# Kernel optimization log

Hardware: AMD Instinct MI355X
Metric: run time of the kernel (lower is better)

The kernel has to match this reference:

```python
import jax, jax.numpy as jnp
import numpy as np

SEGMENT_LENGTHS = [1024, 2048, 4096]
DILATION_RATES = [1, 2, 4]


def setup_inputs() -> dict:
    key = jax.random.key(0)
    kq, kk, kv = jax.random.split(key, 3)
    shape = (2, 4096, 12, 64)  # (batch, seq_len, num_heads, head_dim)
    return {
        "q": jax.random.normal(kq, shape, dtype=jnp.float32),
        "k": jax.random.normal(kk, shape, dtype=jnp.float32),
        "v": jax.random.normal(kv, shape, dtype=jnp.float32),
        "is_causal": 0,
    }


def _group_attention(qg, kg, vg, L, dil_rate, is_causal, scale):
    # qg/kg/vg: [b, n, hg, d]; block-local attention with block size L.
    # NOTE: the original _get_dilated_indices degenerates to the identity
    # segment slice (i=0 row fills all L indices before truncation), so the
    # dilated gather equals the contiguous segment for any dilation_rate.
    b, n, hg, d = qg.shape
    ns = n // L
    q_ = qg.reshape(b, ns, L, hg, d)
    k_ = kg.reshape(b, ns, L, hg, d)
    v_ = vg.reshape(b, ns, L, hg, d)
    scores = jnp.einsum("bsqhd,bskhd->bshqk", q_, k_) * scale  # [b,ns,hg,L,L]
    if is_causal and dil_rate == 1:
        # causal mask is applied only to segment 0 in the original
        causal = jnp.tril(jnp.ones((L, L), dtype=bool))  # [L,L]
        seg0 = (jnp.arange(ns) == 0)[None, :, None, None, None]  # [1,ns,1,1,1]
        neg = jnp.asarray(jnp.finfo(scores.dtype).min, scores.dtype)
        scores = jnp.where(seg0 & ~causal[None, None, None], neg, scores)
    attn = jax.nn.softmax(scores, axis=-1)
    out = jnp.einsum("bshqk,bskhd->bsqhd", attn, v_)
    return out.reshape(b, n, hg, d)


def reference(q, k, v, is_causal):
    b, n, h, d = q.shape
    num_groups = len(SEGMENT_LENGTHS)
    hg = h // num_groups
    scale = 1.0 / (float(d) ** 0.5)
    outs = []
    for gi, (L, r) in enumerate(zip(SEGMENT_LENGTHS, DILATION_RATES)):
        hs = gi * hg
        he = (gi + 1) * hg if gi < num_groups - 1 else h
        outs.append(
            _group_attention(
                q[:, :, hs:he], k[:, :, hs:he], v[:, :, hs:he],
                L, r, bool(is_causal), scale,
            )
        )
    return jnp.concatenate(outs, axis=2)  # [b, n, h, d]
```

## Files before the change

### kernel.cpp

```cpp
#include <hip/hip_runtime.h>
#include <hip/hip_bf16.h>

typedef __bf16 bf16;
typedef _Float16 f16;
typedef __attribute__((ext_vector_type(2))) __bf16 bf16x2;
typedef __attribute__((ext_vector_type(4))) __bf16 bf16x4;
typedef __attribute__((ext_vector_type(8))) __bf16 bf16x8;
typedef __attribute__((ext_vector_type(4))) _Float16 f16x4;
typedef __attribute__((ext_vector_type(8))) _Float16 f16x8;
typedef __attribute__((ext_vector_type(4))) float f32x4;
typedef __attribute__((ext_vector_type(16))) float f32x16;
typedef __attribute__((ext_vector_type(4))) unsigned u32x4;

#define SW(row, col) ((col) ^ (((row) & 7) << 3))

#define GL16(g, l) __builtin_amdgcn_global_load_lds( \
    (const __attribute__((address_space(1))) void*)(g), \
    (__attribute__((address_space(3))) void*)(l), 16, 0, 0)

static __device__ __forceinline__ unsigned pkbf(float a, float b) {
    bf16x2 t = { (bf16)a, (bf16)b };
    return __builtin_bit_cast(unsigned, t);
}

__global__ __launch_bounds__(256) void prep_fused(
    const float* __restrict__ k, const float* __restrict__ v,
    bf16* __restrict__ Kb, bf16* __restrict__ Vt)
{
    __shared__ bf16 T[64][72];
    const int bid = (int)blockIdx.x;
    const int tid = threadIdx.x;
    if (bid < 6144) {
        const size_t i = ((size_t)bid * 256 + tid) * 4;
        float4 f = *(const float4*)(k + i);
        bf16x4 o = { (bf16)f.x, (bf16)f.y, (bf16)f.z, (bf16)f.w };
        *(bf16x4*)(Kb + i) = o;
        return;
    }
    const int vb  = bid - 6144;
    const int n64 = vb & 63;
    const int bh  = vb >> 6;
    const int b   = bh / 12, h = bh - b * 12;
    {
        const int i  = tid >> 2;
        const int dc = (tid & 3) << 4;
        const float* vp = v + (size_t)(b * 4096 + (n64 << 6) + i) * 768 + h * 64 + dc;
        float tv[16];
#pragma unroll
        for (int j2 = 0; j2 < 4; ++j2) *(float4*)&tv[j2 * 4] = ((const float4*)vp)[j2];
#pragma unroll
        for (int j = 0; j < 16; ++j) T[dc + j][i] = (bf16)tv[j];
    }
    __syncthreads();
    {
        const int d  = tid >> 2;
        const int nc = (tid & 3) << 4;
        bf16* op = Vt + (size_t)(bh * 64 + d) * 4096 + (n64 << 6) + nc;
        *(bf16x8*)op       = *(const bf16x8*)&T[d][nc];
        *(bf16x8*)(op + 8) = *(const bf16x8*)&T[d][nc + 8];
    }
}

__global__ __launch_bounds__(256, 3) void attn_kv32(
    const float* __restrict__ q, const bf16* __restrict__ Kb,
    const bf16* __restrict__ Vt, const int* __restrict__ causal_p,
    float* __restrict__ out, f16* __restrict__ Opart, float* __restrict__ lpart)
{
    __shared__ bf16 Ksh[2][32][64];
    __shared__ bf16 Vsh[2][64][32];

    const int tid  = threadIdx.x;
    const int lane = tid & 63;
    const int w    = tid >> 6;
    const int l31  = lane & 31;
    const int h5   = lane >> 5;

    const int bid = (int)blockIdx.x;
    int h, b, qc, so, sp = 0, lbase = 0, oslot = 0;
    bool direct = false, cflag = false;
    if (bid < 1024) {
        h = 8 + (bid >> 8);
        const int r = bid & 255; sp = r >> 6;
        const int r2 = r & 63; b = r2 >> 5; qc = r2 & 31;
        so = sp << 10;
        const int gi = (h - 8) * 64 + b * 32 + qc;
        lbase = gi * 4; oslot = gi * 3 + (sp - 1);
    } else if (bid < 1536) {
        const int i = bid - 1024;
        h = 4 + (i >> 7);
        const int r = i & 127; sp = r >> 6;
        const int r2 = r & 63; b = r2 >> 5; qc = r2 & 31;
        so = ((qc >> 4) << 11) + (sp << 10);
        const int gi = (h - 4) * 64 + b * 32 + qc;
        lbase = 1024 + gi * 2; oslot = 768 + gi;
    } else {
        const int i = bid - 1536;
        h = i >> 6;
        const int r = i & 63; b = r >> 5; qc = r & 31;
        so = (qc >> 3) << 10; direct = true; cflag = true;
    }
    const int q0 = qc << 7;
    const bool causal = cflag && ((qc >> 3) == 0) && (*causal_p != 0);
    const int qg = q0 + (w << 5) + l31;

    const float QS = 0.125f * 1.44269504088896340736f;
    const float* qrp = q + (size_t)(b * 4096 + qg) * 768 + h * 64 + (h5 << 3);
    bf16x8 qf[4];
#pragma unroll
    for (int c = 0; c < 4; ++c) {
        float tq[8];
        *(float4*)&tq[0] = *(const float4*)(qrp + 16 * c);
        *(float4*)&tq[4] = *(const float4*)(qrp + 16 * c + 4);
        bf16x8 t;
#pragma unroll
        for (int j = 0; j < 8; ++j) t[j] = (bf16)(tq[j] * QS);
        qf[c] = t;
    }

    f32x16 o0 = (f32x16)(0.f), o1 = (f32x16)(0.f);
    float lreg = 0.f;

    const int rk  = tid >> 3;
    const int gk  = (tid & 7) ^ (rk & 7);
    const int dv  = tid >> 2;
    const int gv  = (tid & 3) ^ (dv & 3);
    const bf16* kp = Kb + (size_t)(b * 4096 + so + rk) * 768 + h * 64 + gk * 8;
    const bf16* vp = Vt + (size_t)((b * 12 + h) * 64 + dv) * 4096 + so + gv * 8;

    {
        GL16(kp, &Ksh[0][w << 3][0]);
        GL16(vp, &Vsh[0][w << 4][0]);
        kp += 32 * 768; vp += 32;
    }

    for (int t = 0; t < 32; ++t) {
        const int buf = t & 1;
        __builtin_amdgcn_s_barrier();
        if (t < 31) {
            GL16(kp, &Ksh[buf ^ 1][w << 3][0]);
            GL16(vp, &Vsh[buf ^ 1][w << 4][0]);
            kp += 32 * 768; vp += 32;
            asm volatile("s_waitcnt vmcnt(2)" ::: "memory");
        } else {
            asm volatile("s_waitcnt vmcnt(0)" ::: "memory");
        }
        __builtin_amdgcn_s_barrier();

        const bf16 (*Kc)[64] = Ksh[buf];
        const bf16 (*Vc)[32] = Vsh[buf];

        f32x16 s0 = (f32x16)(-12.0f);
        __builtin_amdgcn_s_setprio(1);
#pragma unroll
        for (int c = 0; c < 4; ++c) {
            const int col = (c << 4) + (h5 << 3);
            bf16x8 kf = *(const bf16x8*)&Kc[l31][SW(l31, col)];
            s0 = __builtin_amdgcn_mfma_f32_32x32x16_bf16(kf, qf[c], s0, 0, 0, 0);
        }
        __builtin_amdgcn_s_setprio(0);

        if (causal) {
#pragma unroll
            for (int reg = 0; reg < 16; ++reg) {
                const int kr = (reg & 3) + ((reg >> 2) << 3) + (h5 << 2);
                if (so + (t << 5) + kr > qg) s0[reg] = -1e30f;
            }
        }

        float rs0 = 0.f, rs1 = 0.f;
#pragma unroll
        for (int reg = 0; reg < 16; ++reg) {
            s0[reg] = __builtin_amdgcn_exp2f(s0[reg]);
            if (reg & 1) rs1 += s0[reg]; else rs0 += s0[reg];
        }
        lreg += rs0 + rs1;

        unsigned pk[4][2];
#pragma unroll
        for (int g = 0; g < 4; ++g) {
            pk[g][0] = pkbf(s0[4 * g + 0], s0[4 * g + 1]);
            pk[g][1] = pkbf(s0[4 * g + 2], s0[4 * g + 3]);
        }
        bf16x8 pf[2];
#pragma unroll
        for (int c = 0; c < 2; ++c) {
            unsigned X0 = pk[2 * c][0],     X1 = pk[2 * c][1];
            unsigned Y0 = pk[2 * c + 1][0], Y1 = pk[2 * c + 1][1];
            asm("v_permlane32_swap_b32 %0, %1" : "+v"(X0), "+v"(Y0));
            asm("v_permlane32_swap_b32 %0, %1" : "+v"(X1), "+v"(Y1));
            u32x4 fu = { X0, X1, Y0, Y1 };
            pf[c] = __builtin_bit_cast(bf16x8, fu);
        }

        __builtin_amdgcn_s_setprio(1);
#pragma unroll
        for (int c = 0; c < 2; ++c) {
            const int col = (c << 4) + (h5 << 3);
            bf16x8 vf0 = *(const bf16x8*)&Vc[l31][col ^ ((l31 & 3) << 3)];
            bf16x8 vf1 = *(const bf16x8*)&Vc[32 + l31][col ^ ((l31 & 3) << 3)];
            o0 = __builtin_amdgcn_mfma_f32_32x32x16_bf16(vf0, pf[c], o0, 0, 0, 0);
            o1 = __builtin_amdgcn_mfma_f32_32x32x16_bf16(vf1, pf[c], o1, 0, 0, 0);
        }
        __builtin_amdgcn_s_setprio(0);
    }

    const float lt = lreg + __shfl_xor(lreg, 32);
    const int qloc = (w << 5) + l31;
    if (direct) {
        const float inv = 1.0f / lt;
        float* op = out + (size_t)(b * 4096 + q0 + qloc) * 768 + h * 64;
#pragma unroll
        for (int rr = 0; rr < 4; ++rr) {
            const int d0 = (rr << 3) + (h5 << 2);
            float4 a = { o0[4 * rr] * inv, o0[4 * rr + 1] * inv, o0[4 * rr + 2] * inv, o0[4 * rr + 3] * inv };
            float4 c = { o1[4 * rr] * inv, o1[4 * rr + 1] * inv, o1[4 * rr + 2] * inv, o1[4 * rr + 3] * inv };
            *(float4*)&op[d0]      = a;
            *(float4*)&op[32 + d0] = c;
        }
    } else {
        if (h5 == 0) lpart[(size_t)(lbase + sp) * 128 + qloc] = lt;
        if (sp == 0) {
            float* op = out + (size_t)(b * 4096 + q0 + qloc) * 768 + h * 64;
#pragma unroll
            for (int rr = 0; rr < 4; ++rr) {
                const int d0 = (rr << 3) + (h5 << 2);
                float4 a = { o0[4 * rr], o0[4 * rr + 1], o0[4 * rr + 2], o0[4 * rr + 3] };
                float4 c = { o1[4 * rr], o1[4 * rr + 1], o1[4 * rr + 2], o1[4 * rr + 3] };
                *(float4*)&op[d0]      = a;
                *(float4*)&op[32 + d0] = c;
            }
        } else {
            f16* os = Opart + (size_t)oslot * 8192 + qloc * 64;
#pragma unroll
            for (int rr = 0; rr < 4; ++rr) {
                const int d0 = (rr << 3) + (h5 << 2);
                f16x4 a = { (f16)o0[4 * rr], (f16)o0[4 * rr + 1], (f16)o0[4 * rr + 2], (f16)o0[4 * rr + 3] };
                f16x4 c = { (f16)o1[4 * rr], (f16)o1[4 * rr + 1], (f16)o1[4 * rr + 2], (f16)o1[4 * rr + 3] };
                *(f16x4*)&os[d0]      = a;
                *(f16x4*)&os[32 + d0] = c;
            }
        }
    }
}

__global__ __launch_bounds__(256) void reduce_multi(
    const f16* __restrict__ Opart, const float* __restrict__ lpart,
    float* __restrict__ out)
{
    const int g = (int)blockIdx.x;
    int h, b, qc, nsp, lbase, sbase, nslots;
    if (g < 256) {
        h = 8 + (g >> 6); b = (g >> 5) & 1; qc = g & 31;
        nsp = 4; lbase = g * 4; sbase = g * 3; nslots = 3;
    } else {
        const int gi = g - 256;
        h = 4 + (gi >> 6); b = (gi >> 5) & 1; qc = gi & 31;
        nsp = 2; lbase = 1024 + gi * 2; sbase = 768 + gi; nslots = 1;
    }
    const int t = threadIdx.x;
    const int row = t >> 1;
    const int dh = (t & 1) << 5;
    float l = 0.f;
    for (int s = 0; s < nsp; ++s) l += lpart[(size_t)(lbase + s) * 128 + row];
    const float inv = 1.0f / l;
    float* op = out + (size_t)(b * 4096 + (qc << 7) + row) * 768 + h * 64 + dh;
#pragma unroll
    for (int j = 0; j < 32; j += 8) {
        float acc[8];
        float4 a0 = *(const float4*)(op + j);
        float4 a1 = *(const float4*)(op + j + 4);
        acc[0] = a0.x; acc[1] = a0.y; acc[2] = a0.z; acc[3] = a0.w;
        acc[4] = a1.x; acc[5] = a1.y; acc[6] = a1.z; acc[7] = a1.w;
        for (int s = 0; s < nslots; ++s) {
            f16x8 c = *(const f16x8*)(Opart + (size_t)(sbase + s) * 8192 + row * 64 + dh + j);
#pragma unroll
            for (int e = 0; e < 8; ++e) acc[e] += (float)c[e];
        }
        float4 r0 = { acc[0] * inv, acc[1] * inv, acc[2] * inv, acc[3] * inv };
        float4 r1 = { acc[4] * inv, acc[5] * inv, acc[6] * inv, acc[7] * inv };
        *(float4*)(op + j)     = r0;
        *(float4*)(op + j + 4) = r1;
    }
}

__global__ __launch_bounds__(256, 3) void dila_attn32(
    const float* __restrict__ q, const bf16* __restrict__ Kb,
    const bf16* __restrict__ Vt, const int* __restrict__ causal_p,
    float* __restrict__ out, f16* __restrict__ Opart, float* __restrict__ lpart)
{
    __shared__ bf16 Ksh[2][64][64];
    __shared__ bf16 Vsh[2][64][64];

    const int tid  = threadIdx.x;
    const int lane = tid & 63;
    const int w    = tid >> 6;
    const int l31  = lane & 31;
    const int h5   = lane >> 5;

    const int bid = (int)blockIdx.x;
    int h, b, qc, so, nt, sp = 0, gslot = -1;
    bool cflag = false;
    if (bid < 512) {
        h = 8 + (bid >> 7);
        const int r = bid & 127; sp = r >> 6;
        const int r2 = r & 63; b = r2 >> 5; qc = r2 & 31;
        so = sp << 11; nt = 32;
        gslot = (h - 8) * 64 + b * 32 + qc;
    } else if (bid < 768) {
        const int i = bid - 512;
        h = 4 + (i >> 6);
        const int r = i & 63; b = r >> 5; qc = r & 31;
        so = (qc >> 4) << 11; nt = 32;
    } else {
        const int i = bid - 768;
        h = i >> 7;
        const int r = i & 127; sp = r >> 6;
        const int r2 = r & 63; b = r2 >> 5; qc = r2 & 31;
        so = ((qc >> 3) << 10) + (sp << 9); nt = 8; cflag = true;
        gslot = 256 + h * 64 + b * 32 + qc;
    }
    const int q0 = qc << 7;
    const bool causal = cflag && ((qc >> 3) == 0) && (*causal_p != 0);
    const int qg = q0 + (w << 5) + l31;

    const float QS = 0.125f * 1.44269504088896340736f;
    const float* qrp = q + (size_t)(b * 4096 + qg) * 768 + h * 64 + (h5 << 3);
    bf16x8 qf[4];
#pragma unroll
    for (int c = 0; c < 4; ++c) {
        float tq[8];
        *(float4*)&tq[0] = *(const float4*)(qrp + 16 * c);
        *(float4*)&tq[4] = *(const float4*)(qrp + 16 * c + 4);
        bf16x8 t;
#pragma unroll
        for (int j = 0; j < 8; ++j) t[j] = (bf16)(tq[j] * QS);
        qf[c] = t;
    }

    f32x16 o0 = (f32x16)(0.f), o1 = (f32x16)(0.f);
    float lreg = 0.f;

    const int rK = lane >> 3;
    const int gK = (lane & 7) ^ rK;
    const bf16* kp = Kb + (size_t)(b * 4096 + so + (w << 4) + rK) * 768 + h * 64 + gK * 8;
    const bf16* vp = Vt + (size_t)((b * 12 + h) * 64 + (w << 4) + rK) * 4096 + so + gK * 8;

    {
        bf16* kd = &Ksh[0][w << 4][0];
        bf16* vd = &Vsh[0][w << 4][0];
        GL16(kp, kd); GL16(kp + 8 * 768, kd + 512);
        GL16(vp, vd); GL16(vp + 8 * 4096, vd + 512);
        kp += 64 * 768; vp += 64;
    }

    for (int t = 0; t < nt; ++t) {
        const int buf = t & 1;
        __builtin_amdgcn_s_barrier();
        if (t + 1 < nt) {
            bf16* kd = &Ksh[buf ^ 1][w << 4][0];
            bf16* vd = &Vsh[buf ^ 1][w << 4][0];
            GL16(kp, kd); GL16(kp + 8 * 768, kd + 512);
            GL16(vp, vd); GL16(vp + 8 * 4096, vd + 512);
            kp += 64 * 768; vp += 64;
            asm volatile("s_waitcnt vmcnt(4)" ::: "memory");
        } else {
            asm volatile("s_waitcnt vmcnt(0)" ::: "memory");
        }
        __builtin_amdgcn_s_barrier();

        const bf16 (*Kc)[64] = Ksh[buf];
        const bf16 (*Vc)[64] = Vsh[buf];

        f32x16 s0 = (f32x16)(-12.0f), s1 = (f32x16)(-12.0f);
        __builtin_amdgcn_s_setprio(1);
#pragma unroll
        for (int c = 0; c < 4; ++c) {
            const int col = (c << 4) + (h5 << 3);
            bf16x8 kf0 = *(const bf16x8*)&Kc[l31][SW(l31, col)];
            bf16x8 kf1 = *(const bf16x8*)&Kc[32 + l31][SW(32 + l31, col)];
            s0 = __builtin_amdgcn_mfma_f32_32x32x16_bf16(kf0, qf[c], s0, 0, 0, 0);
            s1 = __builtin_amdgcn_mfma_f32_32x32x16_bf16(kf1, qf[c], s1, 0, 0, 0);
        }
        __builtin_amdgcn_s_setprio(0);

        if (causal) {
#pragma unroll
            for (int reg = 0; reg < 16; ++reg) {
                const int kr = (reg & 3) + ((reg >> 2) << 3) + (h5 << 2);
                if (so + (t << 6) + kr > qg)      s0[reg] = -1e30f;
                if (so + (t << 6) + 32 + kr > qg) s1[reg] = -1e30f;
            }
        }

        float p0[16], p1[16], rs = 0.f;
#pragma unroll
        for (int reg = 0; reg < 16; ++reg) {
            p0[reg] = __builtin_amdgcn_exp2f(s0[reg]);
            p1[reg] = __builtin_amdgcn_exp2f(s1[reg]);
            rs += p0[reg] + p1[reg];
        }
        lreg += rs;

        unsigned pk[8][2];
#pragma unroll
        for (int rr = 0; rr < 4; ++rr) {
            pk[rr][0]     = pkbf(p0[4 * rr + 0], p0[4 * rr + 1]);
            pk[rr][1]     = pkbf(p0[4 * rr + 2], p0[4 * rr + 3]);
            pk[4 + rr][0] = pkbf(p1[4 * rr + 0], p1[4 * rr + 1]);
            pk[4 + rr][1] = pkbf(p1[4 * rr + 2], p1[4 * rr + 3]);
        }
        bf16x8 pf[4];
#pragma unroll
        for (int c = 0; c < 4; ++c) {
            unsigned X0 = pk[2 * c][0],     X1 = pk[2 * c][1];
            unsigned Y0 = pk[2 * c + 1][0], Y1 = pk[2 * c + 1][1];
            asm("v_permlane32_swap_b32 %0, %1" : "+v"(X0), "+v"(Y0));
            asm("v_permlane32_swap_b32 %0, %1" : "+v"(X1), "+v"(Y1));
            u32x4 fu = { X0, X1, Y0, Y1 };
            pf[c] = __builtin_bit_cast(bf16x8, fu);
        }

        __builtin_amdgcn_s_setprio(1);
#pragma unroll
        for (int c = 0; c < 4; ++c) {
            const int col = (c << 4) + (h5 << 3);
            bf16x8 vf0 = *(const bf16x8*)&Vc[l31][SW(l31, col)];
            bf16x8 vf1 = *(const bf16x8*)&Vc[32 + l31][SW(32 + l31, col)];
            o0 = __builtin_amdgcn_mfma_f32_32x32x16_bf16(vf0, pf[c], o0, 0, 0, 0);
            o1 = __builtin_amdgcn_mfma_f32_32x32x16_bf16(vf1, pf[c], o1, 0, 0, 0);
        }
        __builtin_amdgcn_s_setprio(0);
    }

    const float lt = lreg + __shfl_xor(lreg, 32);
    const int qloc = (w << 5) + l31;
    if (gslot < 0) {
        const float inv = 1.0f / lt;
        float* op = out + (size_t)(b * 4096 + q0 + qloc) * 768 + h * 64;
#pragma unroll
        for (int rr = 0; rr < 4; ++rr) {
            const int d0 = (rr << 3) + (h5 << 2);
            float4 a = { o0[4 * rr] * inv, o0[4 * rr + 1] * inv, o0[4 * rr + 2] * inv, o0[4 * rr + 3] * inv };
            float4 c = { o1[4 * rr] * inv, o1[4 * rr + 1] * inv, o1[4 * rr + 2] * inv, o1[4 * rr + 3] * inv };
            *(float4*)&op[d0]      = a;
            *(float4*)&op[32 + d0] = c;
        }
    } else if (sp == 0) {
        float* op = out + (size_t)(b * 4096 + q0 + qloc) * 768 + h * 64;
#pragma unroll
        for (int rr = 0; rr < 4; ++rr) {
            const int d0 = (rr << 3) + (h5 << 2);
            float4 a = { o0[4 * rr], o0[4 * rr + 1], o0[4 * rr + 2], o0[4 * rr + 3] };
            float4 c = { o1[4 * rr], o1[4 * rr + 1], o1[4 * rr + 2], o1[4 * rr + 3] };
            *(float4*)&op[d0]      = a;
            *(float4*)&op[32 + d0] = c;
        }
        if (h5 == 0) lpart[gslot * 256 + qloc] = lt;
    } else {
        f16* os = Opart + (size_t)gslot * 8192 + qloc * 64;
#pragma unroll
        for (int rr = 0; rr < 4; ++rr) {
            const int d0 = (rr << 3) + (h5 << 2);
            f16x4 a = { (f16)o0[4 * rr], (f16)o0[4 * rr + 1], (f16)o0[4 * rr + 2], (f16)o0[4 * rr + 3] };
            f16x4 c = { (f16)o1[4 * rr], (f16)o1[4 * rr + 1], (f16)o1[4 * rr + 2], (f16)o1[4 * rr + 3] };
            *(f16x4*)&os[d0]      = a;
            *(f16x4*)&os[32 + d0] = c;
        }
        if (h5 == 0) lpart[gslot * 256 + 128 + qloc] = lt;
    }
}

__global__ __launch_bounds__(256) void reduce_splits(
    const f16* __restrict__ Opart, const float* __restrict__ lpart,
    float* __restrict__ out)
{
    const int g = (int)blockIdx.x;
    int h, b, qc;
    if (g < 256) { h = 8 + (g >> 6); b = (g >> 5) & 1; qc = g & 31; }
    else { const int g2 = g - 256; h = g2 >> 6; b = (g2 >> 5) & 1; qc = g2 & 31; }
    const int t = threadIdx.x;
    const int row = t >> 1;
    const int dh = (t & 1) << 5;
    const f16* s1 = Opart + (size_t)g * 8192 + row * 64 + dh;
    const float inv = 1.0f / (lpart[g * 256 + row] + lpart[g * 256 + 128 + row]);
    float* op = out + (size_t)(b * 4096 + (qc << 7) + row) * 768 + h * 64 + dh;
#pragma unroll
    for (int j = 0; j < 32; j += 8) {
        float4 a0 = *(const float4*)(op + j);
        float4 a1 = *(const float4*)(op + j + 4);
        f16x8 c = *(const f16x8*)(s1 + j);
        float4 r0 = { (a0.x + (float)c[0]) * inv, (a0.y + (float)c[1]) * inv,
                      (a0.z + (float)c[2]) * inv, (a0.w + (float)c[3]) * inv };
        float4 r1 = { (a1.x + (float)c[4]) * inv, (a1.y + (float)c[5]) * inv,
                      (a1.z + (float)c[6]) * inv, (a1.w + (float)c[7]) * inv };
        *(float4*)(op + j)     = r0;
        *(float4*)(op + j + 4) = r1;
    }
}

__global__ __launch_bounds__(256) void dila_attn_legacy(
    const float* __restrict__ q, const float* __restrict__ k,
    const float* __restrict__ v, const int* __restrict__ causal_p,
    float* __restrict__ out)
{
    __shared__ bf16 Ksh[64][64];
    __shared__ bf16 Vsh[64][64];
    __shared__ bf16 Psh[4][16][72];

    const int tid  = threadIdx.x;
    const int lane = tid & 63;
    const int wid  = tid >> 6;
    const int lm   = lane & 15;
    const int lg   = lane >> 4;

    const int h   = 11 - (int)(blockIdx.x >> 7);
    const int rem = (int)(blockIdx.x & 127);
    const int b   = rem >> 6;
    const int qb  = rem & 63;

    const int grp = h >> 2;
    const int L   = 1024 << grp;
    const int q0  = qb << 6;
    const int seg = q0 / L;
    const int kv0 = seg * L;
    const int nt  = L >> 6;
    const bool causal = (grp == 0) && (seg == 0) && (*causal_p != 0);

    const float* qb_p = q   + (size_t)b * 4096 * 768 + h * 64;
    const float* kb_p = k   + (size_t)b * 4096 * 768 + h * 64;
    const float* vb_p = v   + (size_t)b * 4096 * 768 + h * 64;
    float*       ob_p = out + (size_t)b * 4096 * 768 + h * 64;

    const float QSCALE = 0.125f * 1.44269504088896340736f;
    const int qrow = q0 + (wid << 4) + lm;
    const float* qp = qb_p + (size_t)qrow * 768 + (lg << 3);
    bf16x8 qf[2];
#pragma unroll
    for (int kc = 0; kc < 2; ++kc) {
        float tq[8];
        *(float4*)&tq[0] = ((const float4*)(qp + kc * 32))[0];
        *(float4*)&tq[4] = ((const float4*)(qp + kc * 32))[1];
        bf16x8 tt;
#pragma unroll
        for (int j = 0; j < 8; ++j) tt[j] = (bf16)(tq[j] * QSCALE);
        qf[kc] = tt;
    }

    f32x4 o[4];
#pragma unroll
    for (int i = 0; i < 4; ++i) o[i] = (f32x4){0.f, 0.f, 0.f, 0.f};
    float mrun = -1e30f, lrun = 0.f;

    const int sr = tid >> 2;
    const int sc = (tid & 3) << 4;
    const int vbr = tid >> 4;
    const int vbc = tid & 15;

    const float* kp0 = kb_p + (size_t)(kv0 + sr) * 768 + sc;
    const float* vp0 = vb_p + (size_t)(kv0 + (vbr << 2)) * 768 + (vbc << 2);

    for (int t = 0; t < nt; ++t) {
        {
            const float* kp = kp0 + (size_t)t * (64 * 768);
            float tk[16];
#pragma unroll
            for (int i = 0; i < 4; ++i) *(float4*)&tk[4 * i] = ((const float4*)kp)[i];
            bf16x8 c0, c1;
#pragma unroll
            for (int j = 0; j < 8; ++j) { c0[j] = (bf16)tk[j]; c1[j] = (bf16)tk[8 + j]; }
            *(bf16x8*)&Ksh[sr][SW(sr, sc)]     = c0;
            *(bf16x8*)&Ksh[sr][SW(sr, sc + 8)] = c1;
        }
        {
            const float* vp = vp0 + (size_t)t * (64 * 768);
            float4 tv[4];
#pragma unroll
            for (int i = 0; i < 4; ++i) tv[i] = *(const float4*)(vp + (size_t)i * 768);
#pragma unroll
            for (int jc = 0; jc < 4; ++jc) {
                const int d = (vbc << 2) + jc;
                bf16x4 wv = { (bf16)((&tv[0].x)[jc]), (bf16)((&tv[1].x)[jc]),
                              (bf16)((&tv[2].x)[jc]), (bf16)((&tv[3].x)[jc]) };
                *(bf16x4*)&Vsh[d][SW(d, vbr << 2)] = wv;
            }
        }
        __syncthreads();

        f32x4 s[4];
#pragma unroll
        for (int cb = 0; cb < 4; ++cb) {
            f32x4 acc = (f32x4){0.f, 0.f, 0.f, 0.f};
            const int krow = (cb << 4) + lm;
#pragma unroll
            for (int kc = 0; kc < 2; ++kc) {
                bf16x8 kf = *(const bf16x8*)&Ksh[krow][SW(krow, (lg << 3) + (kc << 5))];
                acc = __builtin_amdgcn_mfma_f32_16x16x32_bf16(kf, qf[kc], acc, 0, 0, 0);
            }
            s[cb] = acc;
        }

        if (causal) {
            const int qg = q0 + (wid << 4) + lm;
#pragma unroll
            for (int cb = 0; cb < 4; ++cb) {
                const int kbase = kv0 + (t << 6) + (cb << 4) + (lg << 2);
#pragma unroll
                for (int r = 0; r < 4; ++r)
                    if (kbase + r > qg) s[cb][r] = -1e30f;
            }
        }

        {
            float mx = fmaxf(fmaxf(fmaxf(s[0][0], s[0][1]), fmaxf(s[0][2], s[0][3])),
                             fmaxf(fmaxf(s[1][0], s[1][1]), fmaxf(s[1][2], s[1][3])));
            float mx2 = fmaxf(fmaxf(fmaxf(s[2][0], s[2][1]), fmaxf(s[2][2], s[2][3])),
                              fmaxf(fmaxf(s[3][0], s[3][1]), fmaxf(s[3][2], s[3][3])));
            mx = fmaxf(mx, mx2);
            mx = fmaxf(mx, __shfl_xor(mx, 16));
            mx = fmaxf(mx, __shfl_xor(mx, 32));
            const float mn = fmaxf(mrun, mx);
            const float cr = __builtin_amdgcn_exp2f(mrun - mn);
            mrun = mn;
            float rs = 0.f;
#pragma unroll
            for (int cb = 0; cb < 4; ++cb) {
                f32x4 pp;
#pragma unroll
                for (int r = 0; r < 4; ++r) {
                    pp[r] = __builtin_amdgcn_exp2f(s[cb][r] - mn);
                    rs += pp[r];
                }
                bf16x4 wv = { (bf16)pp[0], (bf16)pp[1], (bf16)pp[2], (bf16)pp[3] };
                *(bf16x4*)&Psh[wid][lm][(cb << 4) + (lg << 2)] = wv;
            }
            rs += __shfl_xor(rs, 16);
            rs += __shfl_xor(rs, 32);
            lrun = lrun * cr + rs;
#pragma unroll
            for (int db = 0; db < 4; ++db)
#pragma unroll
                for (int r = 0; r < 4; ++r) o[db][r] *= cr;
        }

        {
            bf16x8 pfr[2];
#pragma unroll
            for (int kc = 0; kc < 2; ++kc)
                pfr[kc] = *(const bf16x8*)&Psh[wid][lm][(lg << 3) + (kc << 5)];
#pragma unroll
            for (int db = 0; db < 4; ++db) {
                const int vr = (db << 4) + lm;
#pragma unroll
                for (int kc = 0; kc < 2; ++kc) {
                    bf16x8 vf = *(const bf16x8*)&Vsh[vr][SW(vr, (lg << 3) + (kc << 5))];
                    o[db] = __builtin_amdgcn_mfma_f32_16x16x32_bf16(vf, pfr[kc], o[db], 0, 0, 0);
                }
            }
        }
        __syncthreads();
    }

    {
        const float inv = 1.0f / lrun;
        const int orow = q0 + (wid << 4) + lm;
        float* op = ob_p + (size_t)orow * 768 + (lg << 2);
#pragma unroll
        for (int db = 0; db < 4; ++db) {
            float4 wv = { o[db][0] * inv, o[db][1] * inv, o[db][2] * inv, o[db][3] * inv };
            *(float4*)(op + (db << 4)) = wv;
        }
    }
}

extern "C" void kernel_launch(void* const* d_in, const int* in_sizes, int n_in,
                              void* d_out, int out_size, void* d_ws, size_t ws_size,
                              hipStream_t stream) {
    const float* q = (const float*)d_in[0];
    const float* k = (const float*)d_in[1];
    const float* v = (const float*)d_in[2];
    const int* causal_p = (const int*)d_in[3];
    float* out = (float*)d_out;

    const size_t elems = (size_t)2 * 4096 * 12 * 64;
    const size_t kb_b  = elems * sizeof(bf16);
    const size_t vt_b  = elems * sizeof(bf16);

    const size_t opP_b = (size_t)1024 * 8192 * sizeof(f16);
    const size_t lpP_b = (size_t)1536 * 128 * sizeof(float);
    const size_t needP = kb_b + vt_b + opP_b + lpP_b;

    const size_t opF_b = (size_t)512 * 8192 * sizeof(f16);
    const size_t lpF_b = (size_t)512 * 256 * sizeof(float);
    const size_t needF = kb_b + vt_b + opF_b + lpF_b;

    if (ws_size >= needP) {
        bf16* Kb    = (bf16*)d_ws;
        bf16* Vt    = Kb + elems;
        f16*  Opart = (f16*)(Vt + elems);
        float* lpart = (float*)((char*)Opart + opP_b);
        prep_fused<<<dim3(7680), dim3(256), 0, stream>>>(k, v, Kb, Vt);
        attn_kv32<<<dim3(1792), dim3(256), 0, stream>>>(q, Kb, Vt, causal_p, out, Opart, lpart);
        reduce_multi<<<dim3(512), dim3(256), 0, stream>>>(Opart, lpart, out);
    } else if (ws_size >= needF) {
        bf16* Kb    = (bf16*)d_ws;
        bf16* Vt    = Kb + elems;
        f16*  Opart = (f16*)(Vt + elems);
        float* lpart = (float*)((char*)Opart + opF_b);
        prep_fused<<<dim3(7680), dim3(256), 0, stream>>>(k, v, Kb, Vt);
        dila_attn32<<<dim3(1280), dim3(256), 0, stream>>>(q, Kb, Vt, causal_p, out, Opart, lpart);
        reduce_splits<<<dim3(512), dim3(256), 0, stream>>>(Opart, lpart, out);
    } else {
        dila_attn_legacy<<<dim3(1536), dim3(256), 0, stream>>>(q, k, v, causal_p, out);
    }
}
```

Measured before the change: 114.2 us.

## Pre-pack K/V into MFMA fragment layout and drop LDS staging in attention

The prep kernel now writes K and V in a layout already arranged as per-lane MFMA operand fragments. The attention kernel can then load its operands straight from global memory with one contiguous 16-byte load per lane, and it no longer needs the LDS double buffer or its barriers. Each iteration now covers 64 keys instead of 32, which doubles the MFMA work per step and halves the loop count. The cost is that every wave fetches K and V from global or L2 on its own instead of sharing them through LDS. The V packing also uses scalar strided loads, which may make the prep kernel slower.

```diff
diff --git a/kernel.cpp b/kernel.cpp
--- a/kernel.cpp
+++ b/kernel.cpp
@@ -23,52 +23,52 @@
     return __builtin_bit_cast(unsigned, t);
 }
 
-__global__ __launch_bounds__(256) void prep_fused(
+__global__ __launch_bounds__(256) void prep_pack(
     const float* __restrict__ k, const float* __restrict__ v,
-    bf16* __restrict__ Kb, bf16* __restrict__ Vt)
+    bf16* __restrict__ K2, bf16* __restrict__ V2)
 {
-    __shared__ bf16 T[64][72];
     const int bid = (int)blockIdx.x;
     const int tid = threadIdx.x;
-    if (bid < 6144) {
-        const size_t i = ((size_t)bid * 256 + tid) * 4;
-        float4 f = *(const float4*)(k + i);
-        bf16x4 o = { (bf16)f.x, (bf16)f.y, (bf16)f.z, (bf16)f.w };
-        *(bf16x4*)(Kb + i) = o;
-        return;
-    }
-    const int vb  = bid - 6144;
-    const int n64 = vb & 63;
-    const int bh  = vb >> 6;
-    const int b   = bh / 12, h = bh - b * 12;
-    {
-        const int i  = tid >> 2;
-        const int dc = (tid & 3) << 4;
-        const float* vp = v + (size_t)(b * 4096 + (n64 << 6) + i) * 768 + h * 64 + dc;
-        float tv[16];
-#pragma unroll
-        for (int j2 = 0; j2 < 4; ++j2) *(float4*)&tv[j2 * 4] = ((const float4*)vp)[j2];
-#pragma unroll
-        for (int j = 0; j < 16; ++j) T[dc + j][i] = (bf16)tv[j];
-    }
-    __syncthreads();
-    {
-        const int d  = tid >> 2;
-        const int nc = (tid & 3) << 4;
-        bf16* op = Vt + (size_t)(bh * 64 + d) * 4096 + (n64 << 6) + nc;
-        *(bf16x8*)op       = *(const bf16x8*)&T[d][nc];
-        *(bf16x8*)(op + 8) = *(const bf16x8*)&T[d][nc + 8];
-    }
-}
-
-__global__ __launch_bounds__(256, 3) void attn_kv32(
-    const float* __restrict__ q, const bf16* __restrict__ Kb,
-    const bf16* __restrict__ Vt, const int* __restrict__ causal_p,
+    const bool isV = bid >= 1536;
+    const int id = isV ? bid - 1536 : bid;
+    const int t  = id & 63;
+    const int bh = id >> 6;
+    const int b  = bh / 12, h = bh - b * 12;
+    const size_t dstbase = ((size_t)bh * 64 + t) * 4096;
+#pragma unroll
+    for (int uu = 0; uu < 2; ++uu) {
+        const int u   = tid + uu * 256;
+        const int fid = u >> 6, ln = u & 63;
+        const int l31 = ln & 31, hh = ln >> 5;
+        bf16x8 o;
+        if (!isV) {
+            const int c = fid >> 1, sub = fid & 1;
+            const int n = t * 64 + sub * 32 + l31;
+            const int d = c * 16 + hh * 8;
+            const float* sp = k + (size_t)(b * 4096 + n) * 768 + h * 64 + d;
+            float tf[8];
+            *(float4*)&tf[0] = ((const float4*)sp)[0];
+            *(float4*)&tf[4] = ((const float4*)sp)[1];
+#pragma unroll
+            for (int j = 0; j < 8; ++j) o[j] = (bf16)tf[j];
+            *(bf16x8*)(K2 + dstbase + (size_t)fid * 512 + ln * 8) = o;
+        } else {
+            const int c = fid >> 1, dsub = fid & 1;
+            const int d = dsub * 32 + l31;
+            const int n0 = t * 64 + c * 16 + hh * 8;
+#pragma unroll
+            for (int j = 0; j < 8; ++j)
+                o[j] = (bf16)v[(size_t)(b * 4096 + n0 + j) * 768 + h * 64 + d];
+            *(bf16x8*)(V2 + dstbase + (size_t)fid * 512 + ln * 8) = o;
+        }
+    }
+}
+
+__global__ __launch_bounds__(256, 3) void attn_pack(
+    const float* __restrict__ q, const bf16* __restrict__ K2,
+    const bf16* __restrict__ V2, const int* __restrict__ causal_p,
     float* __restrict__ out, f16* __restrict__ Opart, float* __restrict__ lpart)
 {
-    __shared__ bf16 Ksh[2][32][64];
-    __shared__ bf16 Vsh[2][64][32];
-
     const int tid  = threadIdx.x;
     const int lane = tid & 63;
     const int w    = tid >> 6;
@@ -120,70 +120,52 @@
     f32x16 o0 = (f32x16)(0.f), o1 = (f32x16)(0.f);
     float lreg = 0.f;
 
-    const int rk  = tid >> 3;
-    const int gk  = (tid & 7) ^ (rk & 7);
-    const int dv  = tid >> 2;
-    const int gv  = (tid & 3) ^ (dv & 3);
-    const bf16* kp = Kb + (size_t)(b * 4096 + so + rk) * 768 + h * 64 + gk * 8;
-    const bf16* vp = Vt + (size_t)((b * 12 + h) * 64 + dv) * 4096 + so + gv * 8;
-
-    {
-        GL16(kp, &Ksh[0][w << 3][0]);
-        GL16(vp, &Vsh[0][w << 4][0]);
-        kp += 32 * 768; vp += 32;
-    }
-
-    for (int t = 0; t < 32; ++t) {
-        const int buf = t & 1;
-        __builtin_amdgcn_s_barrier();
-        if (t < 31) {
-            GL16(kp, &Ksh[buf ^ 1][w << 3][0]);
-            GL16(vp, &Vsh[buf ^ 1][w << 4][0]);
-            kp += 32 * 768; vp += 32;
-            asm volatile("s_waitcnt vmcnt(2)" ::: "memory");
-        } else {
-            asm volatile("s_waitcnt vmcnt(0)" ::: "memory");
-        }
-        __builtin_amdgcn_s_barrier();
-
-        const bf16 (*Kc)[64] = Ksh[buf];
-        const bf16 (*Vc)[32] = Vsh[buf];
-
-        f32x16 s0 = (f32x16)(-12.0f);
+    const size_t tbase = ((size_t)(b * 12 + h) * 64 + (so >> 6)) * 4096;
+    const bf16* kt = K2 + tbase + lane * 8;
+    const bf16* vt = V2 + tbase + lane * 8;
+
+    for (int t = 0; t < 16; ++t) {
+        f32x16 s0 = (f32x16)(-12.0f), s1 = (f32x16)(-12.0f);
         __builtin_amdgcn_s_setprio(1);
 #pragma unroll
         for (int c = 0; c < 4; ++c) {
-            const int col = (c << 4) + (h5 << 3);
-            bf16x8 kf = *(const bf16x8*)&Kc[l31][SW(l31, col)];
-            s0 = __builtin_amdgcn_mfma_f32_32x32x16_bf16(kf, qf[c], s0, 0, 0, 0);
+            bf16x8 kf0 = *(const bf16x8*)(kt + (size_t)(c * 2 + 0) * 512);
+            bf16x8 kf1 = *(const bf16x8*)(kt + (size_t)(c * 2 + 1) * 512);
+            s0 = __builtin_amdgcn_mfma_f32_32x32x16_bf16(kf0, qf[c], s0, 0, 0, 0);
+            s1 = __builtin_amdgcn_mfma_f32_32x32x16_bf16(kf1, qf[c], s1, 0, 0, 0);
         }
         __builtin_amdgcn_s_setprio(0);
+        kt += 4096;
 
         if (causal) {
 #pragma unroll
             for (int reg = 0; reg < 16; ++reg) {
                 const int kr = (reg & 3) + ((reg >> 2) << 3) + (h5 << 2);
-                if (so + (t << 5) + kr > qg) s0[reg] = -1e30f;
-            }
-        }
-
-        float rs0 = 0.f, rs1 = 0.f;
+                if (so + (t << 6) + kr > qg)      s0[reg] = -1e30f;
+                if (so + (t << 6) + 32 + kr > qg) s1[reg] = -1e30f;
+            }
+        }
+
+        float p0[16], p1[16], rs = 0.f;
 #pragma unroll
         for (int reg = 0; reg < 16; ++reg) {
-            s0[reg] = __builtin_amdgcn_exp2f(s0[reg]);
-            if (reg & 1) rs1 += s0[reg]; else rs0 += s0[reg];
-        }
-        lreg += rs0 + rs1;
-
-        unsigned pk[4][2];
-#pragma unroll
-        for (int g = 0; g < 4; ++g) {
-            pk[g][0] = pkbf(s0[4 * g + 0], s0[4 * g + 1]);
-            pk[g][1] = pkbf(s0[4 * g + 2], s0[4 * g + 3]);
-        }
-        bf16x8 pf[2];
-#pragma unroll
-        for (int c = 0; c < 2; ++c) {
+            p0[reg] = __builtin_amdgcn_exp2f(s0[reg]);
+            p1[reg] = __builtin_amdgcn_exp2f(s1[reg]);
+            rs += p0[reg] + p1[reg];
+        }
+        lreg += rs;
+
+        unsigned pk[8][2];
+#pragma unroll
+        for (int rr = 0; rr < 4; ++rr) {
+            pk[rr][0]     = pkbf(p0[4 * rr + 0], p0[4 * rr + 1]);
+            pk[rr][1]     = pkbf(p0[4 * rr + 2], p0[4 * rr + 3]);
+            pk[4 + rr][0] = pkbf(p1[4 * rr + 0], p1[4 * rr + 1]);
+            pk[4 + rr][1] = pkbf(p1[4 * rr + 2], p1[4 * rr + 3]);
+        }
+        bf16x8 pf[4];
+#pragma unroll
+        for (int c = 0; c < 4; ++c) {
             unsigned X0 = pk[2 * c][0],     X1 = pk[2 * c][1];
             unsigned Y0 = pk[2 * c + 1][0], Y1 = pk[2 * c + 1][1];
             asm("v_permlane32_swap_b32 %0, %1" : "+v"(X0), "+v"(Y0));
@@ -194,14 +176,14 @@
 
         __builtin_amdgcn_s_setprio(1);
 #pragma unroll
-        for (int c = 0; c < 2; ++c) {
-            const int col = (c << 4) + (h5 << 3);
-            bf16x8 vf0 = *(const bf16x8*)&Vc[l31][col ^ ((l31 & 3) << 3)];
-            bf16x8 vf1 = *(const bf16x8*)&Vc[32 + l31][col ^ ((l31 & 3) << 3)];
+        for (int c = 0; c < 4; ++c) {
+            bf16x8 vf0 = *(const bf16x8*)(vt + (size_t)(c * 2 + 0) * 512);
+            bf16x8 vf1 = *(const bf16x8*)(vt + (size_t)(c * 2 + 1) * 512);
             o0 = __builtin_amdgcn_mfma_f32_32x32x16_bf16(vf0, pf[c], o0, 0, 0, 0);
             o1 = __builtin_amdgcn_mfma_f32_32x32x16_bf16(vf1, pf[c], o1, 0, 0, 0);
         }
         __builtin_amdgcn_s_setprio(0);
+        vt += 4096;
     }
 
     const float lt = lreg + __shfl_xor(lreg, 32);
@@ -280,6 +262,44 @@
         float4 r1 = { acc[4] * inv, acc[5] * inv, acc[6] * inv, acc[7] * inv };
         *(float4*)(op + j)     = r0;
         *(float4*)(op + j + 4) = r1;
+    }
+}
+
+__global__ __launch_bounds__(256) void prep_fused(
+    const float* __restrict__ k, const float* __restrict__ v,
+    bf16* __restrict__ Kb, bf16* __restrict__ Vt)
+{
+    __shared__ bf16 T[64][72];
+    const int bid = (int)blockIdx.x;
+    const int tid = threadIdx.x;
+    if (bid < 6144) {
+        const size_t i = ((size_t)bid * 256 + tid) * 4;
+        float4 f = *(const float4*)(k + i);
+        bf16x4 o = { (bf16)f.x, (bf16)f.y, (bf16)f.z, (bf16)f.w };
+        *(bf16x4*)(Kb + i) = o;
+        return;
+    }
+    const int vb  = bid - 6144;
+    const int n64 = vb & 63;
+    const int bh  = vb >> 6;
+    const int b   = bh / 12, h = bh - b * 12;
+    {
+        const int i  = tid >> 2;
+        const int dc = (tid & 3) << 4;
+        const float* vp = v + (size_t)(b * 4096 + (n64 << 6) + i) * 768 + h * 64 + dc;
+        float tv[16];
+#pragma unroll
+        for (int j2 = 0; j2 < 4; ++j2) *(float4*)&tv[j2 * 4] = ((const float4*)vp)[j2];
+#pragma unroll
+        for (int j = 0; j < 16; ++j) T[dc + j][i] = (bf16)tv[j];
+    }
+    __syncthreads();
+    {
+        const int d  = tid >> 2;
+        const int nc = (tid & 3) << 4;
+        bf16* op = Vt + (size_t)(bh * 64 + d) * 4096 + (n64 << 6) + nc;
+        *(bf16x8*)op       = *(const bf16x8*)&T[d][nc];
+        *(bf16x8*)(op + 8) = *(const bf16x8*)&T[d][nc + 8];
     }
 }
 
@@ -694,12 +714,12 @@
     const size_t needF = kb_b + vt_b + opF_b + lpF_b;
 
     if (ws_size >= needP) {
-        bf16* Kb    = (bf16*)d_ws;
-        bf16* Vt    = Kb + elems;
-        f16*  Opart = (f16*)(Vt + elems);
+        bf16* K2    = (bf16*)d_ws;
+        bf16* V2    = K2 + elems;
+        f16*  Opart = (f16*)(V2 + elems);
         float* lpart = (float*)((char*)Opart + opP_b);
-        prep_fused<<<dim3(7680), dim3(256), 0, stream>>>(k, v, Kb, Vt);
-        attn_kv32<<<dim3(1792), dim3(256), 0, stream>>>(q, Kb, Vt, causal_p, out, Opart, lpart);
+        prep_pack<<<dim3(3072), dim3(256), 0, stream>>>(k, v, K2, V2);
+        attn_pack<<<dim3(1792), dim3(256), 0, stream>>>(q, K2, V2, causal_p, out, Opart, lpart);
         reduce_multi<<<dim3(512), dim3(256), 0, stream>>>(Opart, lpart, out);
     } else if (ws_size >= needF) {
         bf16* Kb    = (bf16*)d_ws;
```

Result: slower. 156.3 us (+36.8%).

## Double KV tile to 64 keys per iteration with precomputed swizzled LDS offsets

Applied to the files above, without the earlier changes.

The attention kernel now processes 64 keys per loop iteration instead of 32, halving the number of iterations and barrier pairs. K and V shared tiles become 64x64 with a common swizzled layout, so precomputed byte offsets serve both the QK and PV fragment loads. Each iteration issues two MFMA chains for scores and four PV steps, which amortizes sync and load-issue overhead over more work. The cost is doubled LDS use (32 KB per block) and more live registers, which may reduce occupancy under the 3-blocks bound.

```diff
diff --git a/kernel.cpp b/kernel.cpp
--- a/kernel.cpp
+++ b/kernel.cpp
@@ -61,13 +61,13 @@
     }
 }
 
-__global__ __launch_bounds__(256, 3) void attn_kv32(
+__global__ __launch_bounds__(256, 3) void attn_eq(
     const float* __restrict__ q, const bf16* __restrict__ Kb,
     const bf16* __restrict__ Vt, const int* __restrict__ causal_p,
     float* __restrict__ out, f16* __restrict__ Opart, float* __restrict__ lpart)
 {
-    __shared__ bf16 Ksh[2][32][64];
-    __shared__ bf16 Vsh[2][64][32];
+    __shared__ bf16 Ksh[2][64][64];
+    __shared__ bf16 Vsh[2][64][64];
 
     const int tid  = threadIdx.x;
     const int lane = tid & 63;
@@ -118,44 +118,62 @@
     }
 
     f32x16 o0 = (f32x16)(0.f), o1 = (f32x16)(0.f);
+    f32x16 C0 = (f32x16)(-12.0f);
     float lreg = 0.f;
 
-    const int rk  = tid >> 3;
-    const int gk  = (tid & 7) ^ (rk & 7);
-    const int dv  = tid >> 2;
-    const int gv  = (tid & 3) ^ (dv & 3);
-    const bf16* kp = Kb + (size_t)(b * 4096 + so + rk) * 768 + h * 64 + gk * 8;
-    const bf16* vp = Vt + (size_t)((b * 12 + h) * 64 + dv) * 4096 + so + gv * 8;
+    unsigned loff[8];
+#pragma unroll
+    for (int c = 0; c < 4; ++c) {
+        const int col = (c << 4) + (h5 << 3);
+        loff[2 * c + 0] = (unsigned)((l31 * 64 + SW(l31, col)) * 2);
+        loff[2 * c + 1] = (unsigned)(((32 + l31) * 64 + SW(32 + l31, col)) * 2);
+    }
+    const char* KB0 = (const char*)&Ksh[0][0][0];
+    const char* VB0 = (const char*)&Vsh[0][0][0];
+
+    const int rK = lane >> 3;
+    const int gK = (lane & 7) ^ rK;
+    const bf16* kp = Kb + (size_t)(b * 4096 + so + (w << 4) + rK) * 768 + h * 64 + gK * 8;
+    const bf16* vp = Vt + (size_t)((b * 12 + h) * 64 + (w << 4) + rK) * 4096 + so + gK * 8;
 
     {
-        GL16(kp, &Ksh[0][w << 3][0]);
-        GL16(vp, &Vsh[0][w << 4][0]);
-        kp += 32 * 768; vp += 32;
-    }
-
-    for (int t = 0; t < 32; ++t) {
+        bf16* kd = &Ksh[0][w << 4][0];
+        bf16* vd = &Vsh[0][w << 4][0];
+        GL16(kp, kd); GL16(kp + 8 * 768, kd + 512);
+        GL16(vp, vd); GL16(vp + 8 * 4096, vd + 512);
+        kp += 64 * 768; vp += 64;
+    }
+
+    for (int t = 0; t < 16; ++t) {
         const int buf = t & 1;
         __builtin_amdgcn_s_barrier();
-        if (t < 31) {
-            GL16(kp, &Ksh[buf ^ 1][w << 3][0]);
-            GL16(vp, &Vsh[buf ^ 1][w << 4][0]);
-            kp += 32 * 768; vp += 32;
-            asm volatile("s_waitcnt vmcnt(2)" ::: "memory");
+        if (t < 15) {
+            bf16* kd = &Ksh[buf ^ 1][w << 4][0];
+            bf16* vd = &Vsh[buf ^ 1][w << 4][0];
+            GL16(kp, kd); GL16(kp + 8 * 768, kd + 512);
+            GL16(vp, vd); GL16(vp + 8 * 4096, vd + 512);
+            kp += 64 * 768; vp += 64;
+            asm volatile("s_waitcnt vmcnt(4)" ::: "memory");
         } else {
             asm volatile("s_waitcnt vmcnt(0)" ::: "memory");
         }
         __builtin_amdgcn_s_barrier();
 
-        const bf16 (*Kc)[64] = Ksh[buf];
-        const bf16 (*Vc)[32] = Vsh[buf];
-
-        f32x16 s0 = (f32x16)(-12.0f);
+        const unsigned bo = (unsigned)(buf << 13);
+
+        f32x16 s0, s1;
         __builtin_amdgcn_s_setprio(1);
 #pragma unroll
         for (int c = 0; c < 4; ++c) {
-            const int col = (c << 4) + (h5 << 3);
-            bf16x8 kf = *(const bf16x8*)&Kc[l31][SW(l31, col)];
-            s0 = __builtin_amdgcn_mfma_f32_32x32x16_bf16(kf, qf[c], s0, 0, 0, 0);
+            bf16x8 kf0 = *(const bf16x8*)(KB0 + bo + loff[2 * c + 0]);
+            bf16x8 kf1 = *(const bf16x8*)(KB0 + bo + loff[2 * c + 1]);
+            if (c == 0) {
+                s0 = __builtin_amdgcn_mfma_f32_32x32x16_bf16(kf0, qf[0], C0, 0, 0, 0);
+                s1 = __builtin_amdgcn_mfma_f32_32x32x16_bf16(kf1, qf[0], C0, 0, 0, 0);
+            } else {
+                s0 = __builtin_amdgcn_mfma_f32_32x32x16_bf16(kf0, qf[c], s0, 0, 0, 0);
+                s1 = __builtin_amdgcn_mfma_f32_32x32x16_bf16(kf1, qf[c], s1, 0, 0, 0);
+            }
         }
         __builtin_amdgcn_s_setprio(0);
 
@@ -163,7 +181,8 @@
 #pragma unroll
             for (int reg = 0; reg < 16; ++reg) {
                 const int kr = (reg & 3) + ((reg >> 2) << 3) + (h5 << 2);
-                if (so + (t << 5) + kr > qg) s0[reg] = -1e30f;
+                if (so + (t << 6) + kr > qg)      s0[reg] = -1e30f;
+                if (so + (t << 6) + 32 + kr > qg) s1[reg] = -1e30f;
             }
         }
 
@@ -171,19 +190,22 @@
 #pragma unroll
         for (int reg = 0; reg < 16; ++reg) {
             s0[reg] = __builtin_amdgcn_exp2f(s0[reg]);
-            if (reg & 1) rs1 += s0[reg]; else rs0 += s0[reg];
+            s1[reg] = __builtin_amdgcn_exp2f(s1[reg]);
+            rs0 += s0[reg]; rs1 += s1[reg];
         }
         lreg += rs0 + rs1;
 
-        unsigned pk[4][2];
-#pragma unroll
-        for (int g = 0; g < 4; ++g) {
-            pk[g][0] = pkbf(s0[4 * g + 0], s0[4 * g + 1]);
-            pk[g][1] = pkbf(s0[4 * g + 2], s0[4 * g + 3]);
-        }
-        bf16x8 pf[2];
-#pragma unroll
-        for (int c = 0; c < 2; ++c) {
+        unsigned pk[8][2];
+#pragma unroll
+        for (int rr = 0; rr < 4; ++rr) {
+            pk[rr][0]     = pkbf(s0[4 * rr + 0], s0[4 * rr + 1]);
+            pk[rr][1]     = pkbf(s0[4 * rr + 2], s0[4 * rr + 3]);
+            pk[4 + rr][0] = pkbf(s1[4 * rr + 0], s1[4 * rr + 1]);
+            pk[4 + rr][1] = pkbf(s1[4 * rr + 2], s1[4 * rr + 3]);
+        }
+        bf16x8 pf[4];
+#pragma unroll
+        for (int c = 0; c < 4; ++c) {
             unsigned X0 = pk[2 * c][0],     X1 = pk[2 * c][1];
             unsigned Y0 = pk[2 * c + 1][0], Y1 = pk[2 * c + 1][1];
             asm("v_permlane32_swap_b32 %0, %1" : "+v"(X0), "+v"(Y0));
@@ -194,10 +216,9 @@
 
         __builtin_amdgcn_s_setprio(1);
 #pragma unroll
-        for (int c = 0; c < 2; ++c) {
-            const int col = (c << 4) + (h5 << 3);
-            bf16x8 vf0 = *(const bf16x8*)&Vc[l31][col ^ ((l31 & 3) << 3)];
-            bf16x8 vf1 = *(const bf16x8*)&Vc[32 + l31][col ^ ((l31 & 3) << 3)];
+        for (int c = 0; c < 4; ++c) {
+            bf16x8 vf0 = *(const bf16x8*)(VB0 + bo + loff[2 * c + 0]);
+            bf16x8 vf1 = *(const bf16x8*)(VB0 + bo + loff[2 * c + 1]);
             o0 = __builtin_amdgcn_mfma_f32_32x32x16_bf16(vf0, pf[c], o0, 0, 0, 0);
             o1 = __builtin_amdgcn_mfma_f32_32x32x16_bf16(vf1, pf[c], o1, 0, 0, 0);
         }
@@ -699,7 +720,7 @@
         f16*  Opart = (f16*)(Vt + elems);
         float* lpart = (float*)((char*)Opart + opP_b);
         prep_fused<<<dim3(7680), dim3(256), 0, stream>>>(k, v, Kb, Vt);
-        attn_kv32<<<dim3(1792), dim3(256), 0, stream>>>(q, Kb, Vt, causal_p, out, Opart, lpart);
+        attn_eq<<<dim3(1792), dim3(256), 0, stream>>>(q, Kb, Vt, causal_p, out, Opart, lpart);
         reduce_multi<<<dim3(512), dim3(256), 0, stream>>>(Opart, lpart, out);
     } else if (ws_size >= needF) {
         bf16* Kb    = (bf16*)d_ws;
```

New measurement: 109.4 us. 1.04x faster.
